# Kernel tuning notes

Measured on AMD Instinct MI355X. Metric: run time of the kernel, lower is better.

Reference implementation:

```python
import jax, jax.numpy as jnp
import numpy as np

B, S, D, H, E, K = 4, 512, 1024, 16, 4, 2
HD = D // H
LN_EPS = 1e-5


def setup_inputs() -> dict:
    key = jax.random.key(0)
    ks = jax.random.split(key, 16)
    def w(k, shape, fan_in):
        return jax.random.normal(k, shape, jnp.float32) / np.float32(np.sqrt(fan_in))
    return {
        "x": jax.random.normal(ks[0], (B, S, D), jnp.float32),
        # stacked per-expert attention params [E, D, D] / [E, D]
        "Wq": w(ks[1], (E, D, D), D), "bq": jnp.zeros((E, D), jnp.float32),
        "Wk": w(ks[2], (E, D, D), D), "bk": jnp.zeros((E, D), jnp.float32),
        "Wv": w(ks[3], (E, D, D), D), "bv": jnp.zeros((E, D), jnp.float32),
        "Wo": w(ks[4], (E, D, D), D), "bo": jnp.zeros((E, D), jnp.float32),
        # router: Linear(D->D/2), LayerNorm, relu, Linear(D/2->E)
        "Wr1": w(ks[5], (D, D // 2), D), "br1": jnp.zeros((D // 2,), jnp.float32),
        "ln_g": jnp.ones((D // 2,), jnp.float32), "ln_b": jnp.zeros((D // 2,), jnp.float32),
        "Wr2": w(ks[6], (D // 2, E), D // 2), "br2": jnp.zeros((E,), jnp.float32),
    }


def _moe_attention(x, Wq, bq, Wk, bk, Wv, bv, Wo, bo, Wr1, br1, ln_g, ln_b, Wr2, br2):
    # ---- router ----
    h = x @ Wr1 + br1                                        # [B,S,D/2]
    mu = jnp.mean(h, axis=-1, keepdims=True)
    var = jnp.var(h, axis=-1, keepdims=True)
    h = (h - mu) * jax.lax.rsqrt(var + LN_EPS) * ln_g + ln_b
    h = jax.nn.relu(h)
    logits = h @ Wr2 + br2                                   # [B,S,E]
    probs = jax.nn.softmax(logits, axis=-1)
    top_p, top_i = jax.lax.top_k(probs, K)                   # [B,S,K]
    # scatter-add of top-k probs into dense expert mask [B,S,E]
    emask = jnp.sum(jax.nn.one_hot(top_i, E, dtype=x.dtype) * top_p[..., None], axis=2)

    # ---- dense per-expert attention (naive: every expert on every token) ----
    def heads(t):  # [E,B,S,D] -> [E,B,H,S,HD]
        return t.reshape(E, B, S, H, HD).transpose(0, 1, 3, 2, 4)

    q = heads(jnp.einsum('bsd,edf->ebsf', x, Wq) + bq[:, None, None, :])
    k = heads(jnp.einsum('bsd,edf->ebsf', x, Wk) + bk[:, None, None, :])
    v = heads(jnp.einsum('bsd,edf->ebsf', x, Wv) + bv[:, None, None, :])

    scores = jnp.einsum('ebhqd,ebhkd->ebhqk', q, k) / np.float32(np.sqrt(HD))
    attn = jax.nn.softmax(scores, axis=-1)                   # [E,B,H,S,S]
    o = jnp.einsum('ebhqk,ebhkd->ebhqd', attn, v)
    o = o.transpose(0, 1, 3, 2, 4).reshape(E, B, S, D)
    o = jnp.einsum('ebsd,edf->ebsf', o, Wo) + bo[:, None, None, :]  # [E,B,S,D]

    # ---- masked combine ----
    return jnp.einsum('ebsd,bse->bsd', o, emask)


def reference(x, Wq, bq, Wk, bk, Wv, bv, Wo, bo, Wr1, br1, ln_g, ln_b, Wr2, br2):
    return _moe_attention(x, Wq, bq, Wk, bk, Wv, bv, Wo, bo,
                          Wr1, br1, ln_g, ln_b, Wr2, br2)
```

## Files before the change

### kernel.cpp

```cpp
#include <hip/hip_runtime.h>
#include <hip/hip_bf16.h>
#include <math.h>

#define B_   4
#define S_   512
#define D_   1024
#define H_   16
#define E_   4
#define HD_  64
#define D2_  512
#define NTOK (B_*S_)

#define TDE ((size_t)NTOK * D_)
#define WWE ((size_t)D_ * D_)
#define ND2 ((size_t)NTOK * D2_)

typedef unsigned short ushort;
typedef short shortv8 __attribute__((ext_vector_type(8)));
typedef ushort ushortv4 __attribute__((ext_vector_type(4)));
typedef _Float16 halfv8 __attribute__((ext_vector_type(8)));
typedef _Float16 halfv4 __attribute__((ext_vector_type(4)));
typedef float floatv4 __attribute__((ext_vector_type(4)));

__device__ __forceinline__ ushort f2bf(float f) {
    union { __hip_bfloat16 b; ushort u; } cv;
    cv.b = __float2bfloat16(f);
    return cv.u;
}
__device__ __forceinline__ float bf2f(ushort u) {
    union { ushort u; __hip_bfloat16 b; } cv;
    cv.u = u;
    return __bfloat162float(cv.b);
}
__device__ __forceinline__ void gload16(const void* g, void* l) {
    __builtin_amdgcn_global_load_lds(
        (const __attribute__((address_space(1))) unsigned int*)g,
        (__attribute__((address_space(3))) unsigned int*)l, 16, 0, 0);
}

__device__ __forceinline__ void gemm_core_bf(
    const ushort* __restrict__ A0, const ushort* __restrict__ A1,
    const ushort* __restrict__ B0, const ushort* __restrict__ B1,
    int K, int klen, int brow, int bcol, ushort* lds, floatv4 acc[4][4])
{
    const int tid  = threadIdx.x;
    const int wave = tid >> 6, lane = tid & 63;
    const int wm = wave >> 1, wn = wave & 1;
    const int lr = lane & 15, lc = lane >> 4;

    const ushort* gsrc[4] = {A0, A1, B0, B1};
    size_t goff[4][2];
    int    loff[4][2];
#pragma unroll
    for (int t = 0; t < 4; t++) {
#pragma unroll
        for (int s = 0; s < 2; s++) {
            int p = s * 256 + tid;
            int m = p >> 2;
            int c = (p & 3) ^ ((m >> 1) & 3);
            int r = (t < 2) ? (brow + m) : (bcol + m);
            goff[t][s] = (size_t)r * K + c * 8;
            loff[t][s] = t * 4096 + p * 8;
        }
    }

    int aoff[4], boff[4];
#pragma unroll
    for (int i = 0; i < 4; i++) {
        int ra = wm * 64 + i * 16 + lr;
        aoff[i] = ra * 32 + ((lc ^ ((ra >> 1) & 3)) * 8);
        int rb2 = wn * 64 + i * 16 + lr;
        boff[i] = rb2 * 32 + ((lc ^ ((rb2 >> 1) & 3)) * 8);
    }

#define STAGEB_(buf, kk) \
    _Pragma("unroll") for (int t = 0; t < 4; t++) \
    _Pragma("unroll") for (int s = 0; s < 2; s++) \
        gload16(gsrc[t] + goff[t][s] + (kk), lds + (buf) * 16384 + loff[t][s]);

    STAGEB_(0, 0)

    int cur = 0;
    for (int k0 = 0; k0 < klen; k0 += 32, cur ^= 1) {
        if (k0 + 32 < klen) {
            STAGEB_(cur ^ 1, k0 + 32)
            asm volatile("s_waitcnt vmcnt(8)" ::: "memory");
        } else {
            asm volatile("s_waitcnt vmcnt(0)" ::: "memory");
        }
        __builtin_amdgcn_s_barrier();
        __builtin_amdgcn_sched_barrier(0);

        const ushort* L = lds + cur * 16384;
        shortv8 ah[4], al[4], bh[4], bl[4];
#pragma unroll
        for (int i = 0; i < 4; i++) {
            ah[i] = *(const shortv8*)(L +         aoff[i]);
            al[i] = *(const shortv8*)(L +  4096 + aoff[i]);
            bh[i] = *(const shortv8*)(L +  8192 + boff[i]);
            bl[i] = *(const shortv8*)(L + 12288 + boff[i]);
        }
#pragma unroll
        for (int mi = 0; mi < 4; mi++)
#pragma unroll
            for (int nj = 0; nj < 4; nj++) {
                acc[mi][nj] = __builtin_amdgcn_mfma_f32_16x16x32_bf16(ah[mi], bh[nj], acc[mi][nj], 0, 0, 0);
                acc[mi][nj] = __builtin_amdgcn_mfma_f32_16x16x32_bf16(ah[mi], bl[nj], acc[mi][nj], 0, 0, 0);
                acc[mi][nj] = __builtin_amdgcn_mfma_f32_16x16x32_bf16(al[mi], bh[nj], acc[mi][nj], 0, 0, 0);
            }

        asm volatile("s_waitcnt lgkmcnt(0)" ::: "memory");
        __builtin_amdgcn_sched_barrier(0);
        __builtin_amdgcn_s_barrier();
    }
#undef STAGEB_
}

template<bool GATHER>
__device__ __forceinline__ void gemm_core_h2(
    const _Float16* __restrict__ A0, const _Float16* __restrict__ B0,
    const int* __restrict__ arow,
    int K, int klen, int brow, int bcol, _Float16* lds, floatv4 acc[8][4])
{
    const int tid  = threadIdx.x;
    const int wave = tid >> 6, lane = tid & 63;
    const int wm = wave >> 1, wn = wave & 1;
    const int lr = lane & 15, lc = lane >> 4;

    size_t goffA[4];
    int    loffA[4];
#pragma unroll
    for (int s = 0; s < 4; s++) {
        int p = s * 256 + tid;
        int m = p >> 2;
        int c = (p & 3) ^ ((m >> 1) & 3);
        int r = GATHER ? (arow[m] & 0xFFFF) : (brow + m);
        goffA[s] = (size_t)r * K + c * 8;
        loffA[s] = p * 8;
    }
    size_t goffB[2];
    int    loffB[2];
#pragma unroll
    for (int s = 0; s < 2; s++) {
        int p = s * 256 + tid;
        int m = p >> 2;
        int c = (p & 3) ^ ((m >> 1) & 3);
        goffB[s] = (size_t)(bcol + m) * K + c * 8;
        loffB[s] = 8192 + p * 8;
    }

    int aoff[8], boff[4];
#pragma unroll
    for (int i = 0; i < 8; i++) {
        int ra = wm * 128 + i * 16 + lr;
        aoff[i] = ra * 32 + ((lc ^ ((ra >> 1) & 3)) * 8);
    }
#pragma unroll
    for (int j = 0; j < 4; j++) {
        int rb = wn * 64 + j * 16 + lr;
        boff[j] = 8192 + rb * 32 + ((lc ^ ((rb >> 1) & 3)) * 8);
    }

#define STAGEH_(buf, kk) \
    _Pragma("unroll") for (int s = 0; s < 4; s++) \
        gload16(A0 + goffA[s] + (kk), lds + (buf) * 12288 + loffA[s]); \
    _Pragma("unroll") for (int s = 0; s < 2; s++) \
        gload16(B0 + goffB[s] + (kk), lds + (buf) * 12288 + loffB[s]);

    STAGEH_(0, 0)

    int cur = 0;
    for (int k0 = 0; k0 < klen; k0 += 32, cur ^= 1) {
        if (k0 + 32 < klen) {
            STAGEH_(cur ^ 1, k0 + 32)
            asm volatile("s_waitcnt vmcnt(6)" ::: "memory");
        } else {
            asm volatile("s_waitcnt vmcnt(0)" ::: "memory");
        }
        __builtin_amdgcn_s_barrier();
        __builtin_amdgcn_sched_barrier(0);

        const _Float16* L = lds + cur * 12288;
        halfv8 aa[8], bb[4];
#pragma unroll
        for (int j = 0; j < 4; j++) bb[j] = *(const halfv8*)(L + boff[j]);
#pragma unroll
        for (int i = 0; i < 8; i++) aa[i] = *(const halfv8*)(L + aoff[i]);
#pragma unroll
        for (int mi = 0; mi < 8; mi++)
#pragma unroll
            for (int nj = 0; nj < 4; nj++)
                acc[mi][nj] = __builtin_amdgcn_mfma_f32_16x16x32_f16(aa[mi], bb[nj], acc[mi][nj], 0, 0, 0);

        asm volatile("s_waitcnt lgkmcnt(0)" ::: "memory");
        __builtin_amdgcn_sched_barrier(0);
        __builtin_amdgcn_s_barrier();
    }
#undef STAGEH_
}

#define ACC_INIT4(acc) \
    _Pragma("unroll") for (int i = 0; i < 4; i++) \
    _Pragma("unroll") for (int j = 0; j < 4; j++) \
    _Pragma("unroll") for (int q = 0; q < 4; q++) acc[i][j][q] = 0.f;

#define ACC_INIT8(acc) \
    _Pragma("unroll") for (int i = 0; i < 8; i++) \
    _Pragma("unroll") for (int j = 0; j < 4; j++) \
    _Pragma("unroll") for (int q = 0; q < 4; q++) acc[i][j][q] = 0.f;

#define EPI_VARS \
    const int lane = threadIdx.x & 63, wave = threadIdx.x >> 6; \
    const int wm = wave >> 1, wn = wave & 1, lr = lane & 15, lc = lane >> 4;

__global__ __launch_bounds__(256, 2) void gemm_router(
    const ushort* __restrict__ xh, const ushort* __restrict__ xl,
    const ushort* __restrict__ wr1h, const ushort* __restrict__ wr1l,
    float* __restrict__ hpart)
{
    __shared__ ushort lds[32768];
    floatv4 acc[4][4];
    ACC_INIT4(acc)

    const int lid = blockIdx.x + 4 * (blockIdx.y + 16 * blockIdx.z);
    const int nid = (lid & 7) * 32 + (lid >> 3);
    const int kz = nid >> 6;
    const int rem = nid & 63;
    const int brow = (rem >> 2) * 128, bcol = (rem & 3) * 128;

    const int koff = kz * 256;
    gemm_core_bf(xh + koff, xl + koff, wr1h + koff, wr1l + koff,
                 D_, 256, brow, bcol, lds, acc);

    float* C = hpart + (size_t)kz * ND2;
    EPI_VARS
#pragma unroll
    for (int mi = 0; mi < 4; mi++)
#pragma unroll
        for (int nj = 0; nj < 4; nj++)
#pragma unroll
            for (int i = 0; i < 4; i++) {
                int row = brow + wm * 64 + mi * 16 + lc * 4 + i;
                int col = bcol + wn * 64 + nj * 16 + lr;
                C[(size_t)row * D2_ + col] = acc[mi][nj][i];
            }
}

__global__ __launch_bounds__(256, 2) void gemm_proj(
    const _Float16* __restrict__ xf,
    const _Float16* __restrict__ wth,
    const float* __restrict__ bq, const float* __restrict__ bk, const float* __restrict__ bv,
    const int* __restrict__ idx, const int* __restrict__ meta,
    _Float16* __restrict__ qf, _Float16* __restrict__ kf, _Float16* __restrict__ vf)
{
    __shared__ _Float16 lds[24576];
    const int lid = blockIdx.x + 8 * (blockIdx.y + 8 * blockIdx.z);
    const int nid = (lid & 7) * 96 + (lid >> 3);
    const int z = nid >> 6;
    const int rem = nid & 63;
    const int brow = (rem >> 3) * 256, bcol = (rem & 7) * 128;

    if (z < 8) {
        const int slot = z >> 1, m = z & 1;
        const size_t so = (size_t)slot * TDE;
        const _Float16* Bm = wth + (size_t)(slot * 4 + 1 + m) * WWE;
        const float* bias = ((m == 0) ? bk : bv) + (size_t)slot * D_;
        _Float16* Oo = ((m == 0) ? kf : vf) + so;

        floatv4 acc[8][4];
        ACC_INIT8(acc)
        gemm_core_h2<false>(xf, Bm, nullptr, D_, D_, brow, bcol, lds, acc);

        EPI_VARS
#pragma unroll
        for (int mi = 0; mi < 8; mi++)
#pragma unroll
            for (int nj = 0; nj < 4; nj++)
#pragma unroll
                for (int i = 0; i < 4; i++) {
                    int row = brow + wm * 128 + mi * 16 + lc * 4 + i;
                    int col = bcol + wn * 64 + nj * 16 + lr;
                    Oo[(size_t)row * D_ + col] = (_Float16)(acc[mi][nj][i] + bias[col]);
                }
    } else {
        const int e = z - 8;
        const int pcnt = meta[32 + e];
        const int brow2 = brow;
        if (brow2 >= pcnt) return;
        const int* arow = idx + e * 2048 + brow2;
        const _Float16* Bm = wth + (size_t)(e * 4 + 0) * WWE;
        const float* bias = bq + (size_t)e * D_;
        const size_t so = (size_t)e * TDE;

        floatv4 acc[8][4];
        ACC_INIT8(acc)
        gemm_core_h2<true>(xf, Bm, arow, D_, D_, brow2, bcol, lds, acc);

        EPI_VARS
#pragma unroll
        for (int mi = 0; mi < 8; mi++)
#pragma unroll
            for (int nj = 0; nj < 4; nj++)
#pragma unroll
                for (int i = 0; i < 4; i++) {
                    int row = brow2 + wm * 128 + mi * 16 + lc * 4 + i;
                    int col = bcol + wn * 64 + nj * 16 + lr;
                    qf[so + (size_t)row * D_ + col] =
                        (_Float16)((acc[mi][nj][i] + bias[col]) * 0.125f);
                }
    }
}

__global__ __launch_bounds__(256, 2) void gemm_combine4(
    const _Float16* __restrict__ oh,
    const _Float16* __restrict__ wth,
    const float* __restrict__ bo, const float* __restrict__ emask,
    const int* __restrict__ idx, const int* __restrict__ meta,
    float* __restrict__ out2)
{
    __shared__ _Float16 lds[24576];
    const int lid = blockIdx.x + 8 * (blockIdx.y + 8 * blockIdx.z);
    const int nid = (lid & 7) * 32 + (lid >> 3);
    const int e = nid >> 6;
    const int rem = nid & 63;
    const int brow = (rem >> 3) * 256, bcol = (rem & 7) * 128;

    const int pcnt = meta[32 + e];
    if (brow >= pcnt) return;
    const size_t so = (size_t)e * TDE;
    const _Float16* Bm = wth + (size_t)(e * 4 + 3) * WWE;
    const float* bias = bo + (size_t)e * D_;
    const int* idxe = idx + e * 2048;

    floatv4 acc[8][4];
    ACC_INIT8(acc)
    gemm_core_h2<false>(oh + so, Bm, nullptr, D_, D_, brow, bcol, lds, acc);

    EPI_VARS
#pragma unroll
    for (int mi = 0; mi < 8; mi++)
#pragma unroll
        for (int nj = 0; nj < 4; nj++)
#pragma unroll
            for (int i = 0; i < 4; i++) {
                int srow = brow + wm * 128 + mi * 16 + lc * 4 + i;
                int raw = idxe[srow];
                if (raw >= 0) {
                    int row = raw & 0xFFFF;
                    int rank = (raw >> 30) & 1;
                    float s = emask[(size_t)row * E_ + e];
                    int col = bcol + wn * 64 + nj * 16 + lr;
                    out2[(size_t)rank * TDE + (size_t)row * D_ + col] =
                        s * (acc[mi][nj][i] + bias[col]);
                }
            }
}

__global__ __launch_bounds__(256) void reduce_out(
    const float* __restrict__ out2, float* __restrict__ out)
{
    size_t i = (size_t)blockIdx.x * 256 + threadIdx.x;
    const float4* p = (const float4*)out2;
    float4 a = p[i], b = p[i + TDE / 4];
    float4 r;
    r.x = a.x + b.x;
    r.y = a.y + b.y;
    r.z = a.z + b.z;
    r.w = a.w + b.w;
    ((float4*)out)[i] = r;
}

__global__ __launch_bounds__(256) void build_lists(
    const float* __restrict__ emask, int* __restrict__ idx, int* __restrict__ meta)
{
    const int e = blockIdx.x;
    const int tid = threadIdx.x;
    __shared__ int scan[256];
    __shared__ int runsh;
    if (tid == 0) runsh = 0;
    int* idxe = idx + e * 2048;

    for (int b = 0; b < B_; b++) {
        __syncthreads();
        const int base = runsh;
        int t0 = b * 512 + tid * 2;
        int f0 = (emask[(size_t)t0 * E_ + e] != 0.f) ? 1 : 0;
        int f1 = (emask[(size_t)(t0 + 1) * E_ + e] != 0.f) ? 1 : 0;
        int my = f0 + f1;
        scan[tid] = my;
        __syncthreads();
        for (int off = 1; off < 256; off <<= 1) {
            int v = (tid >= off) ? scan[tid - off] : 0;
            __syncthreads();
            scan[tid] += v;
            __syncthreads();
        }
        int excl = scan[tid] - my;
        int cnt = scan[255];
        if (f0) {
            int rank = 0;
            for (int ep = 0; ep < e; ep++)
                if (emask[(size_t)t0 * E_ + ep] != 0.f) rank = 1;
            idxe[base + excl] = t0 | (rank << 30);
        }
        if (f1) {
            int rank = 0;
            for (int ep = 0; ep < e; ep++)
                if (emask[(size_t)(t0 + 1) * E_ + ep] != 0.f) rank = 1;
            idxe[base + excl + f0] = (t0 + 1) | (rank << 30);
        }
        int plen = (cnt + 63) & ~63;
        for (int i = cnt + tid; i < plen; i += 256)
            idxe[base + i] = (b * 512) | (int)0x80000000;
        if (tid == 0) {
            meta[e * 4 + b] = base;
            meta[16 + e * 4 + b] = plen >> 6;
            runsh = base + plen;
        }
    }
    __syncthreads();
    int total = runsh;
    if (tid == 0) meta[32 + e] = total;
    for (int i = total + tid; i < 2048; i += 256)
        idxe[i] = (int)0x80000000;
}

__global__ __launch_bounds__(256, 3) void attn_all(
    const _Float16* __restrict__ qf_, const _Float16* __restrict__ kf_,
    const _Float16* __restrict__ vf_,
    _Float16* __restrict__ oh_,
    const int* __restrict__ meta)
{
    const int lid = blockIdx.x + 8 * (blockIdx.y + 64 * blockIdx.z);
    const int nid = (lid & 7) * 256 + (lid >> 3);
    const int e = nid >> 9;
    const int rem = nid & 511;
    const int bhid = rem >> 3, qtile = rem & 7;
    const int bb = bhid >> 4, hh = bhid & 15;

    const int ptiles = meta[16 + e * 4 + bb];
    if (qtile >= ptiles) return;
    const int pstart = meta[e * 4 + bb];

    __shared__ _Float16 Kf[4096];
    __shared__ _Float16 Vt[64 * 72];
    __shared__ _Float16 Pw[4][16 * 72];

    const size_t zo = (size_t)e * TDE;
    const int tid = threadIdx.x;
    const int wave = tid >> 6, lane = tid & 63;
    const int lr = lane & 15, lc = lane >> 4;
    const int q0 = pstart + qtile * 64;
    const size_t kvbase = zo + (size_t)bb * S_ * D_ + hh * 64;
    const size_t qobase = zo + hh * 64;

    halfv8 qq[2];
    {
        size_t qoff = qobase + (size_t)(q0 + wave * 16 + lr) * D_ + lc * 8;
        qq[0] = *(const halfv8*)(qf_ + qoff);
        qq[1] = *(const halfv8*)(qf_ + qoff + 32);
    }

    floatv4 ov[4];
    float m4[4], l4[4];
#pragma unroll
    for (int df = 0; df < 4; df++)
#pragma unroll
        for (int i = 0; i < 4; i++) ov[df][i] = 0.f;
#pragma unroll
    for (int i = 0; i < 4; i++) { m4[i] = -3.0e38f; l4[i] = 0.f; }

    for (int kt = 0; kt < S_ / 64; kt++) {
        const int kk0 = kt * 64;
        __syncthreads();

#pragma unroll
        for (int s = 0; s < 2; s++) {
            int p = s * 256 + tid;
            int r = p >> 3;
            int c = (p & 7) ^ (r & 7);
            gload16(kf_ + kvbase + (size_t)(kk0 + r) * D_ + c * 8, Kf + p * 8);
        }
        {
            const _Float16* vsrc = vf_ + kvbase + (size_t)(kk0 + lane) * D_ + wave * 16;
            halfv8 v0 = *(const halfv8*)vsrc;
            halfv8 v1 = *(const halfv8*)(vsrc + 8);
#pragma unroll
            for (int j = 0; j < 8; j++) Vt[(wave * 16 + j) * 72 + lane] = v0[j];
#pragma unroll
            for (int j = 0; j < 8; j++) Vt[(wave * 16 + 8 + j) * 72 + lane] = v1[j];
        }
        __syncthreads();

        floatv4 sc[4];
#pragma unroll
        for (int n = 0; n < 4; n++)
#pragma unroll
            for (int i = 0; i < 4; i++) sc[n][i] = 0.f;
#pragma unroll
        for (int n = 0; n < 4; n++)
#pragma unroll
            for (int ds = 0; ds < 2; ds++) {
                int off = (16 * n + lr) * 64 + (((ds * 4 + lc) ^ (lr & 7)) * 8);
                halfv8 kr = *(const halfv8*)(Kf + off);
                sc[n] = __builtin_amdgcn_mfma_f32_16x16x32_f16(qq[ds], kr, sc[n], 0, 0, 0);
            }

        float tm[4];
#pragma unroll
        for (int i = 0; i < 4; i++)
            tm[i] = fmaxf(fmaxf(sc[0][i], sc[1][i]), fmaxf(sc[2][i], sc[3][i]));
#pragma unroll
        for (int off = 1; off <= 8; off <<= 1)
#pragma unroll
            for (int i = 0; i < 4; i++)
                tm[i] = fmaxf(tm[i], __shfl_xor(tm[i], off));

        float nm[4], sca[4], ps[4];
#pragma unroll
        for (int i = 0; i < 4; i++) {
            nm[i] = fmaxf(m4[i], tm[i]);
            sca[i] = __expf(m4[i] - nm[i]);
            ps[i] = 0.f;
        }
        float pval[4][4];
#pragma unroll
        for (int n = 0; n < 4; n++)
#pragma unroll
            for (int i = 0; i < 4; i++) {
                float p = __expf(sc[n][i] - nm[i]);
                pval[n][i] = p;
                ps[i] += p;
            }
#pragma unroll
        for (int off = 1; off <= 8; off <<= 1)
#pragma unroll
            for (int i = 0; i < 4; i++)
                ps[i] += __shfl_xor(ps[i], off);
#pragma unroll
        for (int i = 0; i < 4; i++) {
            l4[i] = l4[i] * sca[i] + ps[i];
            m4[i] = nm[i];
        }
#pragma unroll
        for (int df = 0; df < 4; df++)
#pragma unroll
            for (int i = 0; i < 4; i++) ov[df][i] *= sca[i];

#pragma unroll
        for (int n = 0; n < 4; n++)
#pragma unroll
            for (int i = 0; i < 4; i++)
                Pw[wave][(lc * 4 + i) * 72 + 16 * n + lr] = (_Float16)pval[n][i];
        __syncthreads();

#pragma unroll
        for (int ks = 0; ks < 2; ks++) {
            halfv8 pa = *(const halfv8*)(&Pw[wave][lr * 72 + ks * 32 + lc * 8]);
#pragma unroll
            for (int df = 0; df < 4; df++) {
                halfv8 vr = *(const halfv8*)(Vt + (df * 16 + lr) * 72 + ks * 32 + lc * 8);
                ov[df] = __builtin_amdgcn_mfma_f32_16x16x32_f16(pa, vr, ov[df], 0, 0, 0);
            }
        }
    }

#pragma unroll
    for (int df = 0; df < 4; df++)
#pragma unroll
        for (int i = 0; i < 4; i++) {
            float val = ov[df][i] / l4[i];
            size_t off = qobase + (size_t)(q0 + wave * 16 + lc * 4 + i) * D_ + df * 16 + lr;
            oh_[off] = (_Float16)val;
        }
}

__global__ __launch_bounds__(256) void split_f32(
    const float* __restrict__ in, ushort* __restrict__ hb, ushort* __restrict__ lb,
    _Float16* __restrict__ hf)
{
    int i = blockIdx.x * 256 + threadIdx.x;
    float4 v = ((const float4*)in)[i];
    float vv[4] = {v.x, v.y, v.z, v.w};
    ushortv4 hv, lv;
    halfv4 hhv;
#pragma unroll
    for (int j = 0; j < 4; j++) {
        ushort h = f2bf(vv[j]);
        hv[j] = h;
        lv[j] = f2bf(vv[j] - bf2f(h));
        hhv[j] = (_Float16)vv[j];
    }
    ((ushortv4*)hb)[i] = hv;
    ((ushortv4*)lb)[i] = lv;
    ((halfv4*)hf)[i] = hhv;
}

__global__ __launch_bounds__(256) void tsplit(
    const float* __restrict__ W, ushort* __restrict__ Th, ushort* __restrict__ Tl,
    int K, int N)
{
    __shared__ float tile[64][65];
    const int n0 = blockIdx.x * 64, k0 = blockIdx.y * 64;
    const int tid = threadIdx.x;
#pragma unroll
    for (int i = 0; i < 16; i++) {
        int idx = i * 256 + tid;
        int r = idx >> 6, c = idx & 63;
        tile[r][c] = W[(size_t)(k0 + r) * N + n0 + c];
    }
    __syncthreads();
#pragma unroll
    for (int i = 0; i < 16; i++) {
        int idx = i * 256 + tid;
        int rn = idx >> 6, ck = idx & 63;
        float v = tile[ck][rn];
        ushort h = f2bf(v);
        Th[(size_t)(n0 + rn) * K + k0 + ck] = h;
        Tl[(size_t)(n0 + rn) * K + k0 + ck] = f2bf(v - bf2f(h));
    }
}

__global__ __launch_bounds__(256) void tsplit16h(
    const float* __restrict__ Wq, const float* __restrict__ Wk,
    const float* __restrict__ Wv, const float* __restrict__ Wo,
    _Float16* __restrict__ Th)
{
    __shared__ float tile[64][65];
    const int mg = blockIdx.z;
    const int e = mg >> 2, m = mg & 3;
    const float* W = ((m == 0) ? Wq : (m == 1) ? Wk : (m == 2) ? Wv : Wo) + (size_t)e * WWE;
    _Float16* T = Th + (size_t)mg * WWE;
    const int n0 = blockIdx.x * 64, k0 = blockIdx.y * 64;
    const int tid = threadIdx.x;
#pragma unroll
    for (int i = 0; i < 16; i++) {
        int idx = i * 256 + tid;
        int r = idx >> 6, c = idx & 63;
        tile[r][c] = W[(size_t)(k0 + r) * D_ + n0 + c];
    }
    __syncthreads();
#pragma unroll
    for (int i = 0; i < 16; i++) {
        int idx = i * 256 + tid;
        int rn = idx >> 6, ck = idx & 63;
        T[(size_t)(n0 + rn) * D_ + k0 + ck] = (_Float16)tile[ck][rn];
    }
}

__global__ __launch_bounds__(256) void router_post(
    const float* __restrict__ hpart, const float* __restrict__ br1,
    const float* __restrict__ ln_g, const float* __restrict__ ln_b,
    const float* __restrict__ Wr2, const float* __restrict__ br2,
    float* __restrict__ emask)
{
    const int t = blockIdx.x;
    const int tid = threadIdx.x;
    __shared__ float red[256];
    __shared__ float logits[E_];

    const float* hp = hpart + (size_t)t * D2_;
    float x0 = hp[tid] + hp[ND2 + tid] + hp[2 * ND2 + tid] + hp[3 * ND2 + tid] + br1[tid];
    float x1 = hp[tid + 256] + hp[ND2 + tid + 256] + hp[2 * ND2 + tid + 256]
             + hp[3 * ND2 + tid + 256] + br1[tid + 256];

    red[tid] = x0 + x1; __syncthreads();
    for (int off = 128; off; off >>= 1) { if (tid < off) red[tid] += red[tid + off]; __syncthreads(); }
    float mu = red[0] * (1.f / 512.f);
    __syncthreads();

    float d0 = x0 - mu, d1 = x1 - mu;
    red[tid] = d0 * d0 + d1 * d1; __syncthreads();
    for (int off = 128; off; off >>= 1) { if (tid < off) red[tid] += red[tid + off]; __syncthreads(); }
    float rs = rsqrtf(red[0] * (1.f / 512.f) + 1e-5f);
    __syncthreads();

    float n0 = fmaxf(fmaf(d0 * rs, ln_g[tid],       ln_b[tid]),       0.f);
    float n1 = fmaxf(fmaf(d1 * rs, ln_g[tid + 256], ln_b[tid + 256]), 0.f);

    for (int e = 0; e < E_; e++) {
        red[tid] = n0 * Wr2[(size_t)tid * E_ + e] + n1 * Wr2[(size_t)(tid + 256) * E_ + e];
        __syncthreads();
        for (int off = 128; off; off >>= 1) { if (tid < off) red[tid] += red[tid + off]; __syncthreads(); }
        if (tid == 0) logits[e] = red[0] + br2[e];
        __syncthreads();
    }

    if (tid == 0) {
        float mx = fmaxf(fmaxf(logits[0], logits[1]), fmaxf(logits[2], logits[3]));
        float p[E_], sum = 0.f;
        for (int e = 0; e < E_; e++) { p[e] = expf(logits[e] - mx); sum += p[e]; }
        float inv = 1.f / sum;
        for (int e = 0; e < E_; e++) p[e] *= inv;
        int i1 = 0;
        for (int e = 1; e < E_; e++) if (p[e] > p[i1]) i1 = e;
        int i2 = -1;
        for (int e = 0; e < E_; e++) { if (e == i1) continue; if (i2 < 0 || p[e] > p[i2]) i2 = e; }
        float o[E_] = {0.f, 0.f, 0.f, 0.f};
        o[i1] = p[i1]; o[i2] = p[i2];
        for (int e = 0; e < E_; e++) emask[(size_t)t * E_ + e] = o[e];
    }
}

extern "C" void kernel_launch(void* const* d_in, const int* in_sizes, int n_in,
                              void* d_out, int out_size, void* d_ws, size_t ws_size,
                              hipStream_t stream) {
    const float* x   = (const float*)d_in[0];
    const float* Wq  = (const float*)d_in[1];
    const float* bq  = (const float*)d_in[2];
    const float* Wk  = (const float*)d_in[3];
    const float* bk  = (const float*)d_in[4];
    const float* Wv  = (const float*)d_in[5];
    const float* bv  = (const float*)d_in[6];
    const float* Wo  = (const float*)d_in[7];
    const float* bo  = (const float*)d_in[8];
    const float* Wr1 = (const float*)d_in[9];
    const float* br1 = (const float*)d_in[10];
    const float* lng = (const float*)d_in[11];
    const float* lnb = (const float*)d_in[12];
    const float* Wr2 = (const float*)d_in[13];
    const float* br2 = (const float*)d_in[14];

    float* out = (float*)d_out;
    char* w = (char*)d_ws;
    dim3 blk(256);
    const size_t MB = 1024ull * 1024ull;

    float*    emask = (float*)w;
    int*      idx   = (int*)(w + 64 * 1024);
    int*      meta  = (int*)(w + 96 * 1024);
    _Float16* wth   = (_Float16*)(w + 1 * MB);
    ushort*   wr1h  = (ushort*)(w + 33 * MB);
    ushort*   wr1l  = (ushort*)(w + 34 * MB);
    ushort*   xh    = (ushort*)(w + 35 * MB);
    ushort*   xl    = (ushort*)(w + 39 * MB);
    _Float16* xfh   = (_Float16*)(w + 43 * MB);
    float*    hpart = (float*)(w + 47 * MB);
    _Float16* qfb   = (_Float16*)(w + 63 * MB);
    _Float16* kfb   = (_Float16*)(w + 79 * MB);
    _Float16* vfb   = (_Float16*)(w + 95 * MB);
    _Float16* ohb   = (_Float16*)(w + 111 * MB);
    float*    out2  = (float*)(w + 127 * MB);

    split_f32<<<dim3(NTOK * D_ / 1024), blk, 0, stream>>>(x, xh, xl, xfh);
    tsplit<<<dim3(D2_ / 64, D_ / 64), blk, 0, stream>>>(Wr1, wr1h, wr1l, D_, D2_);
    tsplit16h<<<dim3(16, 16, 16), blk, 0, stream>>>(Wq, Wk, Wv, Wo, wth);

    gemm_router<<<dim3(D2_ / 128, NTOK / 128, 4), blk, 0, stream>>>(
        xh, xl, wr1h, wr1l, hpart);
    router_post<<<dim3(NTOK), blk, 0, stream>>>(hpart, br1, lng, lnb, Wr2, br2, emask);
    build_lists<<<dim3(E_), blk, 0, stream>>>(emask, idx, meta);

    gemm_proj<<<dim3(8, 8, 12), blk, 0, stream>>>(
        xfh, wth, bq, bk, bv, idx, meta, qfb, kfb, vfb);

    attn_all<<<dim3(S_ / 64, B_ * H_, E_), blk, 0, stream>>>(
        qfb, kfb, vfb, ohb, meta);

    gemm_combine4<<<dim3(8, 8, 4), blk, 0, stream>>>(
        ohb, wth, bo, emask, idx, meta, out2);
    reduce_out<<<dim3(TDE / 1024), blk, 0, stream>>>(out2, out);
}
```

Measured before the change: 225.3 us.

## Merge router and QKV projection GEMMs into one launch and retile attention

The router GEMM and the Q/K/V projections now run in a single launch, with blocks assigned per XCD. Q is computed densely for all tokens, and the token gather moves into the attention kernel's Q load, so projection no longer depends on the routing lists. Attention now processes 128-key tiles with XOR-swizzled LDS layouts, prefetches V into registers for the next tile, drops a barrier before the P·V stage, and raises wave priority around the MFMA sections. The cost is computing Q for every token rather than only routed ones, and more LDS per block.

```diff
diff --git a/kernel.cpp b/kernel.cpp
--- a/kernel.cpp
+++ b/kernel.cpp
@@ -116,10 +116,8 @@
 #undef STAGEB_
 }
 
-template<bool GATHER>
 __device__ __forceinline__ void gemm_core_h2(
     const _Float16* __restrict__ A0, const _Float16* __restrict__ B0,
-    const int* __restrict__ arow,
     int K, int klen, int brow, int bcol, _Float16* lds, floatv4 acc[8][4])
 {
     const int tid  = threadIdx.x;
@@ -134,8 +132,7 @@
         int p = s * 256 + tid;
         int m = p >> 2;
         int c = (p & 3) ^ ((m >> 1) & 3);
-        int r = GATHER ? (arow[m] & 0xFFFF) : (brow + m);
-        goffA[s] = (size_t)r * K + c * 8;
+        goffA[s] = (size_t)(brow + m) * K + c * 8;
         loffA[s] = p * 8;
     }
     size_t goffB[2];
@@ -213,54 +210,47 @@
     const int lane = threadIdx.x & 63, wave = threadIdx.x >> 6; \
     const int wm = wave >> 1, wn = wave & 1, lr = lane & 15, lc = lane >> 4;
 
-__global__ __launch_bounds__(256, 2) void gemm_router(
+__global__ __launch_bounds__(256, 2) void gemm_mega(
     const ushort* __restrict__ xh, const ushort* __restrict__ xl,
     const ushort* __restrict__ wr1h, const ushort* __restrict__ wr1l,
-    float* __restrict__ hpart)
-{
-    __shared__ ushort lds[32768];
-    floatv4 acc[4][4];
-    ACC_INIT4(acc)
-
-    const int lid = blockIdx.x + 4 * (blockIdx.y + 16 * blockIdx.z);
-    const int nid = (lid & 7) * 32 + (lid >> 3);
-    const int kz = nid >> 6;
-    const int rem = nid & 63;
-    const int brow = (rem >> 2) * 128, bcol = (rem & 3) * 128;
-
-    const int koff = kz * 256;
-    gemm_core_bf(xh + koff, xl + koff, wr1h + koff, wr1l + koff,
-                 D_, 256, brow, bcol, lds, acc);
-
-    float* C = hpart + (size_t)kz * ND2;
-    EPI_VARS
-#pragma unroll
-    for (int mi = 0; mi < 4; mi++)
-#pragma unroll
-        for (int nj = 0; nj < 4; nj++)
-#pragma unroll
-            for (int i = 0; i < 4; i++) {
-                int row = brow + wm * 64 + mi * 16 + lc * 4 + i;
-                int col = bcol + wn * 64 + nj * 16 + lr;
-                C[(size_t)row * D2_ + col] = acc[mi][nj][i];
-            }
-}
-
-__global__ __launch_bounds__(256, 2) void gemm_proj(
-    const _Float16* __restrict__ xf,
-    const _Float16* __restrict__ wth,
+    float* __restrict__ hpart,
+    const _Float16* __restrict__ xf, const _Float16* __restrict__ wth,
     const float* __restrict__ bq, const float* __restrict__ bk, const float* __restrict__ bv,
-    const int* __restrict__ idx, const int* __restrict__ meta,
     _Float16* __restrict__ qf, _Float16* __restrict__ kf, _Float16* __restrict__ vf)
 {
-    __shared__ _Float16 lds[24576];
-    const int lid = blockIdx.x + 8 * (blockIdx.y + 8 * blockIdx.z);
-    const int nid = (lid & 7) * 96 + (lid >> 3);
-    const int z = nid >> 6;
-    const int rem = nid & 63;
-    const int brow = (rem >> 3) * 256, bcol = (rem & 7) * 128;
-
-    if (z < 8) {
+    __shared__ ushort smem[32768];
+    const int bid = blockIdx.x;
+    const int xcd = bid & 7, j = bid >> 3;
+
+    if (j < 32) {
+        const int u = xcd * 32 + j;
+        const int kz = u >> 6;
+        const int rem = u & 63;
+        const int brow = (rem >> 2) * 128, bcol = (rem & 3) * 128;
+
+        floatv4 acc[4][4];
+        ACC_INIT4(acc)
+        const int koff = kz * 256;
+        gemm_core_bf(xh + koff, xl + koff, wr1h + koff, wr1l + koff,
+                     D_, 256, brow, bcol, smem, acc);
+
+        float* C = hpart + (size_t)kz * ND2;
+        EPI_VARS
+#pragma unroll
+        for (int mi = 0; mi < 4; mi++)
+#pragma unroll
+            for (int nj = 0; nj < 4; nj++)
+#pragma unroll
+                for (int i = 0; i < 4; i++) {
+                    int row = brow + wm * 64 + mi * 16 + lc * 4 + i;
+                    int col = bcol + wn * 64 + nj * 16 + lr;
+                    C[(size_t)row * D2_ + col] = acc[mi][nj][i];
+                }
+    } else if (j < 96) {
+        const int u = xcd * 64 + (j - 32);
+        const int z = u >> 6;
+        const int rem = u & 63;
+        const int brow = (rem >> 3) * 256, bcol = (rem & 7) * 128;
         const int slot = z >> 1, m = z & 1;
         const size_t so = (size_t)slot * TDE;
         const _Float16* Bm = wth + (size_t)(slot * 4 + 1 + m) * WWE;
@@ -269,7 +259,7 @@
 
         floatv4 acc[8][4];
         ACC_INIT8(acc)
-        gemm_core_h2<false>(xf, Bm, nullptr, D_, D_, brow, bcol, lds, acc);
+        gemm_core_h2(xf, Bm, D_, D_, brow, bcol, (_Float16*)smem, acc);
 
         EPI_VARS
 #pragma unroll
@@ -283,18 +273,17 @@
                     Oo[(size_t)row * D_ + col] = (_Float16)(acc[mi][nj][i] + bias[col]);
                 }
     } else {
-        const int e = z - 8;
-        const int pcnt = meta[32 + e];
-        const int brow2 = brow;
-        if (brow2 >= pcnt) return;
-        const int* arow = idx + e * 2048 + brow2;
+        const int u = xcd * 32 + (j - 96);
+        const int e = u >> 6;
+        const int rem = u & 63;
+        const int brow = (rem >> 3) * 256, bcol = (rem & 7) * 128;
         const _Float16* Bm = wth + (size_t)(e * 4 + 0) * WWE;
         const float* bias = bq + (size_t)e * D_;
-        const size_t so = (size_t)e * TDE;
+        _Float16* Oo = qf + (size_t)e * TDE;
 
         floatv4 acc[8][4];
         ACC_INIT8(acc)
-        gemm_core_h2<true>(xf, Bm, arow, D_, D_, brow2, bcol, lds, acc);
+        gemm_core_h2(xf, Bm, D_, D_, brow, bcol, (_Float16*)smem, acc);
 
         EPI_VARS
 #pragma unroll
@@ -303,9 +292,9 @@
             for (int nj = 0; nj < 4; nj++)
 #pragma unroll
                 for (int i = 0; i < 4; i++) {
-                    int row = brow2 + wm * 128 + mi * 16 + lc * 4 + i;
+                    int row = brow + wm * 128 + mi * 16 + lc * 4 + i;
                     int col = bcol + wn * 64 + nj * 16 + lr;
-                    qf[so + (size_t)row * D_ + col] =
+                    Oo[(size_t)row * D_ + col] =
                         (_Float16)((acc[mi][nj][i] + bias[col]) * 0.125f);
                 }
     }
@@ -334,7 +323,7 @@
 
     floatv4 acc[8][4];
     ACC_INIT8(acc)
-    gemm_core_h2<false>(oh + so, Bm, nullptr, D_, D_, brow, bcol, lds, acc);
+    gemm_core_h2(oh + so, Bm, D_, D_, brow, bcol, lds, acc);
 
     EPI_VARS
 #pragma unroll
@@ -429,7 +418,7 @@
     const _Float16* __restrict__ qf_, const _Float16* __restrict__ kf_,
     const _Float16* __restrict__ vf_,
     _Float16* __restrict__ oh_,
-    const int* __restrict__ meta)
+    const int* __restrict__ idx, const int* __restrict__ meta)
 {
     const int lid = blockIdx.x + 8 * (blockIdx.y + 64 * blockIdx.z);
     const int nid = (lid & 7) * 256 + (lid >> 3);
@@ -442,9 +431,9 @@
     if (qtile >= ptiles) return;
     const int pstart = meta[e * 4 + bb];
 
-    __shared__ _Float16 Kf[4096];
-    __shared__ _Float16 Vt[64 * 72];
-    __shared__ _Float16 Pw[4][16 * 72];
+    __shared__ _Float16 Kf[128 * 64];
+    __shared__ _Float16 Vt[64 * 128];
+    __shared__ _Float16 Pw[4][16 * 128];
 
     const size_t zo = (size_t)e * TDE;
     const int tid = threadIdx.x;
@@ -452,11 +441,12 @@
     const int lr = lane & 15, lc = lane >> 4;
     const int q0 = pstart + qtile * 64;
     const size_t kvbase = zo + (size_t)bb * S_ * D_ + hh * 64;
-    const size_t qobase = zo + hh * 64;
 
     halfv8 qq[2];
     {
-        size_t qoff = qobase + (size_t)(q0 + wave * 16 + lr) * D_ + lc * 8;
+        int slot = q0 + wave * 16 + lr;
+        int tok = idx[e * 2048 + slot] & 0xFFFF;
+        size_t qoff = zo + (size_t)tok * D_ + hh * 64 + lc * 8;
         qq[0] = *(const halfv8*)(qf_ + qoff);
         qq[1] = *(const halfv8*)(qf_ + qoff + 32);
     }
@@ -470,46 +460,66 @@
 #pragma unroll
     for (int i = 0; i < 4; i++) { m4[i] = -3.0e38f; l4[i] = 0.f; }
 
-    for (int kt = 0; kt < S_ / 64; kt++) {
-        const int kk0 = kt * 64;
+    halfv8 vr[2][2];
+#define LOADV_(kk0_) \
+    _Pragma("unroll") for (int pp = 0; pp < 2; pp++) { \
+        const _Float16* vsrc = vf_ + kvbase + (size_t)((kk0_) + pp * 64 + lane) * D_ + wave * 16; \
+        vr[pp][0] = *(const halfv8*)vsrc; \
+        vr[pp][1] = *(const halfv8*)(vsrc + 8); \
+    }
+
+    LOADV_(0)
+
+    for (int kt = 0; kt < S_ / 128; kt++) {
+        const int kk0 = kt * 128;
         __syncthreads();
 
 #pragma unroll
-        for (int s = 0; s < 2; s++) {
+        for (int s = 0; s < 4; s++) {
             int p = s * 256 + tid;
             int r = p >> 3;
             int c = (p & 7) ^ (r & 7);
             gload16(kf_ + kvbase + (size_t)(kk0 + r) * D_ + c * 8, Kf + p * 8);
         }
-        {
-            const _Float16* vsrc = vf_ + kvbase + (size_t)(kk0 + lane) * D_ + wave * 16;
-            halfv8 v0 = *(const halfv8*)vsrc;
-            halfv8 v1 = *(const halfv8*)(vsrc + 8);
-#pragma unroll
-            for (int j = 0; j < 8; j++) Vt[(wave * 16 + j) * 72 + lane] = v0[j];
-#pragma unroll
-            for (int j = 0; j < 8; j++) Vt[(wave * 16 + 8 + j) * 72 + lane] = v1[j];
+#pragma unroll
+        for (int pp = 0; pp < 2; pp++) {
+            int k = pp * 64 + lane;
+            int kc = k >> 3, kl = k & 7;
+#pragma unroll
+            for (int h = 0; h < 2; h++)
+#pragma unroll
+                for (int jj = 0; jj < 8; jj++) {
+                    int d = wave * 16 + h * 8 + jj;
+                    Vt[d * 128 + ((kc ^ jj) << 3) + kl] = vr[pp][h][jj];
+                }
         }
         __syncthreads();
 
-        floatv4 sc[4];
-#pragma unroll
-        for (int n = 0; n < 4; n++)
+        if (kt + 1 < S_ / 128) { LOADV_(kk0 + 128) }
+
+        floatv4 sc[8];
+#pragma unroll
+        for (int n = 0; n < 8; n++)
 #pragma unroll
             for (int i = 0; i < 4; i++) sc[n][i] = 0.f;
-#pragma unroll
-        for (int n = 0; n < 4; n++)
+        __builtin_amdgcn_s_setprio(1);
+#pragma unroll
+        for (int n = 0; n < 8; n++)
 #pragma unroll
             for (int ds = 0; ds < 2; ds++) {
                 int off = (16 * n + lr) * 64 + (((ds * 4 + lc) ^ (lr & 7)) * 8);
                 halfv8 kr = *(const halfv8*)(Kf + off);
                 sc[n] = __builtin_amdgcn_mfma_f32_16x16x32_f16(qq[ds], kr, sc[n], 0, 0, 0);
             }
+        __builtin_amdgcn_s_setprio(0);
 
         float tm[4];
 #pragma unroll
-        for (int i = 0; i < 4; i++)
-            tm[i] = fmaxf(fmaxf(sc[0][i], sc[1][i]), fmaxf(sc[2][i], sc[3][i]));
+        for (int i = 0; i < 4; i++) {
+            float a = fmaxf(fmaxf(sc[0][i], sc[1][i]), fmaxf(sc[2][i], sc[3][i]));
+            float b = fmaxf(fmaxf(sc[4][i], sc[5][i]), fmaxf(sc[6][i], sc[7][i]));
+            tm[i] = fmaxf(a, b);
+        }
 #pragma unroll
         for (int off = 1; off <= 8; off <<= 1)
 #pragma unroll
@@ -523,14 +533,16 @@
             sca[i] = __expf(m4[i] - nm[i]);
             ps[i] = 0.f;
         }
-        float pval[4][4];
-#pragma unroll
-        for (int n = 0; n < 4; n++)
+#pragma unroll
+        for (int n = 0; n < 8; n++)
 #pragma unroll
             for (int i = 0; i < 4; i++) {
                 float p = __expf(sc[n][i] - nm[i]);
-                pval[n][i] = p;
                 ps[i] += p;
+                int q = lc * 4 + i;
+                int kcol = 16 * n + lr;
+                Pw[wave][q * 128 + (((kcol >> 3) ^ (q & 7)) << 3) + (kcol & 7)] =
+                    (_Float16)p;
             }
 #pragma unroll
         for (int off = 1; off <= 8; off <<= 1)
@@ -547,24 +559,25 @@
 #pragma unroll
             for (int i = 0; i < 4; i++) ov[df][i] *= sca[i];
 
-#pragma unroll
-        for (int n = 0; n < 4; n++)
-#pragma unroll
-            for (int i = 0; i < 4; i++)
-                Pw[wave][(lc * 4 + i) * 72 + 16 * n + lr] = (_Float16)pval[n][i];
-        __syncthreads();
-
-#pragma unroll
-        for (int ks = 0; ks < 2; ks++) {
-            halfv8 pa = *(const halfv8*)(&Pw[wave][lr * 72 + ks * 32 + lc * 8]);
+        asm volatile("s_waitcnt lgkmcnt(0)" ::: "memory");
+        __builtin_amdgcn_sched_barrier(0);
+
+        __builtin_amdgcn_s_setprio(1);
+#pragma unroll
+        for (int ks = 0; ks < 4; ks++) {
+            int ch = ((ks * 4 + lc) ^ (lr & 7)) * 8;
+            halfv8 pa = *(const halfv8*)(&Pw[wave][lr * 128 + ch]);
 #pragma unroll
             for (int df = 0; df < 4; df++) {
-                halfv8 vr = *(const halfv8*)(Vt + (df * 16 + lr) * 72 + ks * 32 + lc * 8);
-                ov[df] = __builtin_amdgcn_mfma_f32_16x16x32_f16(pa, vr, ov[df], 0, 0, 0);
+                halfv8 vfr = *(const halfv8*)(Vt + (df * 16 + lr) * 128 + ch);
+                ov[df] = __builtin_amdgcn_mfma_f32_16x16x32_f16(pa, vfr, ov[df], 0, 0, 0);
             }
         }
-    }
-
+        __builtin_amdgcn_s_setprio(0);
+    }
+#undef LOADV_
+
+    const size_t qobase = zo + hh * 64;
 #pragma unroll
     for (int df = 0; df < 4; df++)
 #pragma unroll
@@ -746,16 +759,14 @@
     tsplit<<<dim3(D2_ / 64, D_ / 64), blk, 0, stream>>>(Wr1, wr1h, wr1l, D_, D2_);
     tsplit16h<<<dim3(16, 16, 16), blk, 0, stream>>>(Wq, Wk, Wv, Wo, wth);
 
-    gemm_router<<<dim3(D2_ / 128, NTOK / 128, 4), blk, 0, stream>>>(
-        xh, xl, wr1h, wr1l, hpart);
+    gemm_mega<<<dim3(1024), blk, 0, stream>>>(
+        xh, xl, wr1h, wr1l, hpart, xfh, wth, bq, bk, bv, qfb, kfb, vfb);
+
     router_post<<<dim3(NTOK), blk, 0, stream>>>(hpart, br1, lng, lnb, Wr2, br2, emask);
     build_lists<<<dim3(E_), blk, 0, stream>>>(emask, idx, meta);
 
-    gemm_proj<<<dim3(8, 8, 12), blk, 0, stream>>>(
-        xfh, wth, bq, bk, bv, idx, meta, qfb, kfb, vfb);
-
-    attn_all<<<dim3(S_ / 64, B_ * H_, E_), blk, 0, stream>>>(
-        qfb, kfb, vfb, ohb, meta);
+    attn_all<<<dim3(8, 64, 4), blk, 0, stream>>>(
+        qfb, kfb, vfb, ohb, idx, meta);
 
     gemm_combine4<<<dim3(8, 8, 4), blk, 0, stream>>>(
         ohb, wth, bo, emask, idx, meta, out2);
```

New measurement: 211.3 us. -6.2%, faster.
